# Optimization experiments

Hardware: AMD Instinct MI355X
Metric: run time of the kernel (lower is better)

## Reference

```python
import jax, jax.numpy as jnp
import numpy as np

B, IN_DIM, HID, K, D = 16384, 1024, 2048, 8192, 128
COMMIT = 0.25


def setup_inputs() -> dict:
    key = jax.random.key(0)
    ks = jax.random.split(key, 10)
    s1 = 1.0 / np.sqrt(IN_DIM)
    s2 = 1.0 / np.sqrt(HID)
    s3 = 1.0 / np.sqrt(D)
    return {
        "x": jax.random.uniform(ks[0], (B, IN_DIM), dtype=jnp.float32),
        "W1": jax.random.normal(ks[1], (IN_DIM, HID), dtype=jnp.float32) * s1,
        "b1": jnp.zeros((HID,), jnp.float32),
        "W2": jax.random.normal(ks[2], (HID, D), dtype=jnp.float32) * s2,
        "b2": jnp.zeros((D,), jnp.float32),
        # torch init: uniform(-1/K, 1/K)
        "codebook": jax.random.uniform(ks[3], (K, D), dtype=jnp.float32, minval=-1.0 / K, maxval=1.0 / K),
        "W3": jax.random.normal(ks[4], (D, HID), dtype=jnp.float32) * s3,
        "b3": jnp.zeros((HID,), jnp.float32),
        "W4": jax.random.normal(ks[5], (HID, IN_DIM), dtype=jnp.float32) * s2,
        "b4": jnp.zeros((IN_DIM,), jnp.float32),
    }


def reference(x, W1, b1, W2, b2, codebook, W3, b3, W4, b4):
    # Encoder MLP: [B, IN] -> [B, D]
    h = jax.nn.relu(x @ W1 + b1)
    z = h @ W2 + b2                                   # [B, D]

    # Squared-distance to codebook: ||z||^2 - 2 z C^T + ||C||^2  -> [B, K]
    dists = (jnp.sum(z * z, axis=1, keepdims=True)
             - 2.0 * (z @ codebook.T)
             + jnp.sum(codebook * codebook, axis=1))
    indices = jnp.argmin(dists, axis=1)               # [B]
    z_q = codebook[indices]                            # [B, D]

    # Straight-through estimator
    z_q_st = z + jax.lax.stop_gradient(z_q - z)

    # Decoder MLP: [B, D] -> [B, IN]
    h2 = jax.nn.relu(z_q_st @ W3 + b3)
    recon = jax.nn.sigmoid(h2 @ W4 + b4)

    sg_zq = jax.lax.stop_gradient(z_q)
    mse = jnp.mean(jnp.square(sg_zq - z))
    loss = mse + COMMIT * mse
    return (recon, loss, indices)
```

## Files before the change

kernel.cpp:

```cpp
#include <hip/hip_runtime.h>
#include <hip/hip_bf16.h>


#define B_    16384
#define INDIM 1024
#define HID   2048
#define KCB   8192
#define DDIM  128

#define CAND_CAP 2000000u
#define LBUF_CAP 1024u

typedef __bf16    bf16x8   __attribute__((ext_vector_type(8)));
typedef float     floatx4  __attribute__((ext_vector_type(4)));
typedef double    doublex4 __attribute__((ext_vector_type(4)));
typedef _Float16  half8    __attribute__((ext_vector_type(8)));
typedef __fp16    fp16x2   __attribute__((ext_vector_type(2)));

#define XS 4096.0f
#define WS 8192.0f
#define SCALE_INV 2.9802322387695312e-08

__device__ __forceinline__ unsigned long long pack_key(float d, int code)
{
    unsigned int u = __float_as_uint(d);
    u = (u & 0x80000000u) ? ~u : (u | 0x80000000u);
    return ((unsigned long long)u << 32) | (unsigned int)code;
}

__device__ __forceinline__ float unpack_d(unsigned long long key)
{
    unsigned int u = (unsigned int)(key >> 32);
    u = (u & 0x80000000u) ? (u ^ 0x80000000u) : ~u;
    return __uint_as_float(u);
}

__device__ __forceinline__ void gll16(const float* g, float* l)
{
    __builtin_amdgcn_global_load_lds(
        (const __attribute__((address_space(1))) void*)g,
        (__attribute__((address_space(3))) void*)l, 16, 0, 0);
}

template <int ACT, int PMASK>
__launch_bounds__(256)
__global__ void gemm_split_f16(const float* __restrict__ A, const _Float16* __restrict__ Bs_g,
                               const float* __restrict__ bias, float* __restrict__ Cout,
                               int M, int N, int K)
{
    __shared__ float    As[128 * 32];
    __shared__ _Float16 Bsh[64 * 64];

    const int t    = threadIdx.x;
    const int m0   = blockIdx.y * 128, n0 = blockIdx.x * 64;
    const int wave = t >> 6, lane = t & 63;
    const int wr   = (wave >> 1) * 64, wc = (wave & 1) * 32;
    const int quad = lane >> 4, l16 = lane & 15;
    const int lr   = lane >> 3;
    const int lcA  = ((lane & 7) ^ lr) * 4;
    const int slB  = lane & 7;
    const int lrB  = lane >> 3;

    floatx4  accf[4][2];
    doublex4 accd[4][2];
#pragma unroll
    for (int i = 0; i < 4; ++i)
#pragma unroll
        for (int j = 0; j < 2; ++j) {
            accf[i][j] = (floatx4){0.f, 0.f, 0.f, 0.f};
            accd[i][j] = (doublex4){0.0, 0.0, 0.0, 0.0};
        }

    const int NKT = K >> 5;
    for (int kt = 0; kt < NKT; ++kt) {
        const int k0 = kt << 5;
        __syncthreads();
#pragma unroll
        for (int s = 0; s < 4; ++s) {
            int r = wave * 32 + s * 8;
            gll16(A + (size_t)(m0 + r + lr) * K + k0 + lcA, &As[r * 32]);
        }
#pragma unroll
        for (int s = 0; s < 2; ++s) {
            int rb = wave * 16 + s * 8 + lrB;
            int ccs = slB ^ (lrB & 7);
            gll16((const float*)(Bs_g + (size_t)(n0 + rb) * (2 * K) + kt * 64 + ccs * 8),
                  (float*)&Bsh[(wave * 16 + s * 8) * 64]);
        }
        __syncthreads();

        half8 a1[4], a2[4];
#pragma unroll
        for (int i = 0; i < 4; ++i) {
            const int row = wr + i * 16 + l16;
            const int s0  = (2 * quad) ^ (row & 7);
            const int s1  = (2 * quad + 1) ^ (row & 7);
            floatx4 f0 = *(const floatx4*)&As[row * 32 + s0 * 4];
            floatx4 f1 = *(const floatx4*)&As[row * 32 + s1 * 4];
            union { half8 v; fp16x2 h[4]; } u1, u2;
            float sv[8];
#pragma unroll
            for (int q = 0; q < 4; ++q) sv[q] = f0[q] * XS;
#pragma unroll
            for (int q = 0; q < 4; ++q) sv[4 + q] = f1[q] * XS;
#pragma unroll
            for (int q = 0; q < 4; ++q) {
                fp16x2 hi = __builtin_amdgcn_cvt_pkrtz(sv[2 * q], sv[2 * q + 1]);
                u1.h[q] = hi;
                float r0 = sv[2 * q] - (float)hi[0];
                float r1 = sv[2 * q + 1] - (float)hi[1];
                u2.h[q] = __builtin_amdgcn_cvt_pkrtz(r0, r1);
            }
            a1[i] = u1.v; a2[i] = u2.v;
        }
        half8 b1[2], b2[2];
#pragma unroll
        for (int j = 0; j < 2; ++j) {
            const int row = wc + j * 16 + l16;
            b1[j] = *(const half8*)&Bsh[row * 64 + ((0 + quad) ^ (row & 7)) * 8];
            b2[j] = *(const half8*)&Bsh[row * 64 + ((4 + quad) ^ (row & 7)) * 8];
        }
#pragma unroll
        for (int i = 0; i < 4; ++i)
#pragma unroll
            for (int j = 0; j < 2; ++j)
                accf[i][j] = __builtin_amdgcn_mfma_f32_16x16x32_f16(a1[i], b1[j], accf[i][j], 0, 0, 0);
#pragma unroll
        for (int i = 0; i < 4; ++i)
#pragma unroll
            for (int j = 0; j < 2; ++j)
                accf[i][j] = __builtin_amdgcn_mfma_f32_16x16x32_f16(a1[i], b2[j], accf[i][j], 0, 0, 0);
#pragma unroll
        for (int i = 0; i < 4; ++i)
#pragma unroll
            for (int j = 0; j < 2; ++j)
                accf[i][j] = __builtin_amdgcn_mfma_f32_16x16x32_f16(a2[i], b1[j], accf[i][j], 0, 0, 0);

        if ((kt & PMASK) == PMASK) {
#pragma unroll
            for (int i = 0; i < 4; ++i)
#pragma unroll
                for (int j = 0; j < 2; ++j) {
#pragma unroll
                    for (int r = 0; r < 4; ++r)
                        accd[i][j][r] += (double)accf[i][j][r] * SCALE_INV;
                    accf[i][j] = (floatx4){0.f, 0.f, 0.f, 0.f};
                }
        }
    }
    if (NKT & PMASK) {
#pragma unroll
        for (int i = 0; i < 4; ++i)
#pragma unroll
            for (int j = 0; j < 2; ++j)
#pragma unroll
                for (int r = 0; r < 4; ++r)
                    accd[i][j][r] += (double)accf[i][j][r] * SCALE_INV;
    }

#pragma unroll
    for (int i = 0; i < 4; ++i)
#pragma unroll
        for (int j = 0; j < 2; ++j)
#pragma unroll
            for (int r = 0; r < 4; ++r) {
                int row = m0 + wr + i * 16 + quad * 4 + r;
                int col = n0 + wc + j * 16 + l16;
                float f = (float)(accd[i][j][r] + (double)bias[col]);
                if (ACT == 1) f = fmaxf(f, 0.f);
                Cout[(size_t)row * N + col] = f;
            }
}

__launch_bounds__(256)
__global__ void gemm_split_pre(const _Float16* __restrict__ As_g, const _Float16* __restrict__ Bs_g,
                               const float* __restrict__ bias, float* __restrict__ Cout,
                               int M, int N, int K)
{
    __shared__ _Float16 Ash[128 * 64];
    __shared__ _Float16 Bsh[64 * 64];

    const int t    = threadIdx.x;
    const int m0   = blockIdx.y * 128, n0 = blockIdx.x * 64;
    const int wave = t >> 6, lane = t & 63;
    const int wr   = (wave >> 1) * 64, wc = (wave & 1) * 32;
    const int quad = lane >> 4, l16 = lane & 15;
    const int slB  = lane & 7;
    const int lrB  = lane >> 3;
    const int ccs  = slB ^ (lrB & 7);

    floatx4  accf[4][2];
    doublex4 accd[4][2];
#pragma unroll
    for (int i = 0; i < 4; ++i)
#pragma unroll
        for (int j = 0; j < 2; ++j) {
            accf[i][j] = (floatx4){0.f, 0.f, 0.f, 0.f};
            accd[i][j] = (doublex4){0.0, 0.0, 0.0, 0.0};
        }

    const int NKT = K >> 5;
    for (int kt = 0; kt < NKT; ++kt) {
        __syncthreads();
#pragma unroll
        for (int s = 0; s < 4; ++s) {
            int ra = wave * 32 + s * 8 + lrB;
            gll16((const float*)(As_g + (size_t)(m0 + ra) * (2 * K) + kt * 64 + ccs * 8),
                  (float*)&Ash[(wave * 32 + s * 8) * 64]);
        }
#pragma unroll
        for (int s = 0; s < 2; ++s) {
            int rb = wave * 16 + s * 8 + lrB;
            gll16((const float*)(Bs_g + (size_t)(n0 + rb) * (2 * K) + kt * 64 + ccs * 8),
                  (float*)&Bsh[(wave * 16 + s * 8) * 64]);
        }
        __syncthreads();

        half8 a1[4], a2[4], b1[2], b2[2];
#pragma unroll
        for (int i = 0; i < 4; ++i) {
            const int row = wr + i * 16 + l16;
            a1[i] = *(const half8*)&Ash[row * 64 + ((0 + quad) ^ (row & 7)) * 8];
            a2[i] = *(const half8*)&Ash[row * 64 + ((4 + quad) ^ (row & 7)) * 8];
        }
#pragma unroll
        for (int j = 0; j < 2; ++j) {
            const int row = wc + j * 16 + l16;
            b1[j] = *(const half8*)&Bsh[row * 64 + ((0 + quad) ^ (row & 7)) * 8];
            b2[j] = *(const half8*)&Bsh[row * 64 + ((4 + quad) ^ (row & 7)) * 8];
        }
#pragma unroll
        for (int i = 0; i < 4; ++i)
#pragma unroll
            for (int j = 0; j < 2; ++j)
                accf[i][j] = __builtin_amdgcn_mfma_f32_16x16x32_f16(a1[i], b1[j], accf[i][j], 0, 0, 0);
#pragma unroll
        for (int i = 0; i < 4; ++i)
#pragma unroll
            for (int j = 0; j < 2; ++j)
                accf[i][j] = __builtin_amdgcn_mfma_f32_16x16x32_f16(a1[i], b2[j], accf[i][j], 0, 0, 0);
#pragma unroll
        for (int i = 0; i < 4; ++i)
#pragma unroll
            for (int j = 0; j < 2; ++j)
                accf[i][j] = __builtin_amdgcn_mfma_f32_16x16x32_f16(a2[i], b1[j], accf[i][j], 0, 0, 0);

        if ((kt & 3) == 3) {
#pragma unroll
            for (int i = 0; i < 4; ++i)
#pragma unroll
                for (int j = 0; j < 2; ++j) {
#pragma unroll
                    for (int r = 0; r < 4; ++r)
                        accd[i][j][r] += (double)accf[i][j][r] * SCALE_INV;
                    accf[i][j] = (floatx4){0.f, 0.f, 0.f, 0.f};
                }
        }
    }

#pragma unroll
    for (int i = 0; i < 4; ++i)
#pragma unroll
        for (int j = 0; j < 2; ++j)
#pragma unroll
            for (int r = 0; r < 4; ++r) {
                int row = m0 + wr + i * 16 + quad * 4 + r;
                int col = n0 + wc + j * 16 + l16;
                float f = (float)(accd[i][j][r] + (double)bias[col]);
                f = fmaxf(f, 0.f);
                Cout[(size_t)row * N + col] = f;
            }
}

__global__ void split_x(const float* __restrict__ in, _Float16* __restrict__ outS, int n8)
{
    int i = blockIdx.x * 256 + threadIdx.x;
    if (i >= n8) return;
    const int K = INDIM;
    int m  = i / (K / 8);
    int k8 = i % (K / 8);
    int k  = k8 * 8;
    const float* src = in + (size_t)m * K + k;
    floatx4 f0 = *(const floatx4*)(src);
    floatx4 f1 = *(const floatx4*)(src + 4);
    union { half8 v; fp16x2 h[4]; } u1, u2;
    float sv[8];
#pragma unroll
    for (int q = 0; q < 4; ++q) sv[q] = f0[q] * XS;
#pragma unroll
    for (int q = 0; q < 4; ++q) sv[4 + q] = f1[q] * XS;
#pragma unroll
    for (int q = 0; q < 4; ++q) {
        fp16x2 hi = __builtin_amdgcn_cvt_pkrtz(sv[2 * q], sv[2 * q + 1]);
        u1.h[q] = hi;
        float r0 = sv[2 * q] - (float)hi[0];
        float r1 = sv[2 * q + 1] - (float)hi[1];
        u2.h[q] = __builtin_amdgcn_cvt_pkrtz(r0, r1);
    }
    size_t base = (size_t)m * (2 * K) + (size_t)(k >> 5) * 64 + (k & 31);
    *(half8*)(outS + base)      = u1.v;
    *(half8*)(outS + base + 32) = u2.v;
}

__global__ void transpose_split_f16(const float* __restrict__ in, _Float16* __restrict__ outS,
                                    int K, int N)
{
    __shared__ float tile[32][33];
    int k0 = blockIdx.x * 32, n0 = blockIdx.y * 32;
    int tr = threadIdx.x >> 5, tc = threadIdx.x & 31;
#pragma unroll
    for (int s = 0; s < 4; ++s)
        tile[tr + 8 * s][tc] = in[(size_t)(k0 + tr + 8 * s) * N + n0 + tc];
    __syncthreads();
#pragma unroll
    for (int s = 0; s < 4; ++s) {
        int n = n0 + tr + 8 * s;
        int k = k0 + tc;
        float w = tile[tc][tr + 8 * s] * WS;
        _Float16 p0 = (_Float16)w;
        float r = w - (float)p0;
        _Float16 p1 = (_Float16)r;
        size_t base = (size_t)n * (2 * K) + (size_t)(k >> 5) * 64 + (k & 31);
        outS[base]      = p0;
        outS[base + 32] = p1;
    }
}

__global__ void rownorm_kernel(const float* __restrict__ M, float* __restrict__ nrm)
{
    int k = blockIdx.x * 4 + (threadIdx.x >> 6);
    int lane = threadIdx.x & 63;
    float2 c = *(const float2*)(M + (size_t)k * DDIM + lane * 2);
    float q0 = c.x * c.x;
    float q1 = c.y * c.y;
    double s = (double)q0 + (double)q1;
#pragma unroll
    for (int off = 32; off > 0; off >>= 1) s += __shfl_down(s, off);
    if (lane == 0) nrm[k] = (float)s;
}

__global__ void cnmax_kernel(const float* __restrict__ cn, float* __restrict__ out)
{
    __shared__ float red[4];
    int t = threadIdx.x;
    float m = 0.f;
    for (int i = t; i < KCB; i += 256) m = fmaxf(m, cn[i]);
#pragma unroll
    for (int off = 32; off > 0; off >>= 1) m = fmaxf(m, __shfl_down(m, off));
    if ((t & 63) == 0) red[t >> 6] = m;
    __syncthreads();
    if (t == 0) out[0] = fmaxf(fmaxf(red[0], red[1]), fmaxf(red[2], red[3]));
}

__global__ void cvt_half(const float* __restrict__ in, _Float16* __restrict__ out,
                         float scale, int n8)
{
    int i = blockIdx.x * 256 + threadIdx.x;
    if (i >= n8) return;
    const float4 a = *(const float4*)(in + (size_t)i * 8);
    const float4 b = *(const float4*)(in + (size_t)i * 8 + 4);
    half8 h;
    h[0] = (_Float16)(a.x * scale); h[1] = (_Float16)(a.y * scale);
    h[2] = (_Float16)(a.z * scale); h[3] = (_Float16)(a.w * scale);
    h[4] = (_Float16)(b.x * scale); h[5] = (_Float16)(b.y * scale);
    h[6] = (_Float16)(b.z * scale); h[7] = (_Float16)(b.w * scale);
    *(half8*)(out + (size_t)i * 8) = h;
}

template <int EMIT>
__launch_bounds__(256)
__global__ void score_sweep2(const _Float16* __restrict__ zh, const _Float16* __restrict__ ch,
                             const float* __restrict__ nz32, const float* __restrict__ cn32,
                             unsigned long long* __restrict__ gbestA,
                             const float* __restrict__ cnmaxp,
                             unsigned* __restrict__ listCnt, unsigned* __restrict__ list)
{
    __shared__ __align__(16) _Float16 Zs[32 * 128];
    __shared__ __align__(16) _Float16 Cs[128 * 128];
    __shared__ unsigned long long best[32];
    __shared__ unsigned lbuf[LBUF_CAP];
    __shared__ unsigned lcnt, lbase;

    const int t    = threadIdx.x;
    const int m0   = blockIdx.x * 32;
    const int wave = t >> 6, lane = t & 63;
    const int quad = lane >> 4, l16 = lane & 15;
    const int srow = lane >> 4, sc = lane & 15;

    if (EMIT == 0) { if (t < 32) best[t] = ~0ull; }
    else if (t == 0) lcnt = 0u;

#pragma unroll
    for (int s = 0; s < 2; ++s) {
        const int rbase = s * 16 + wave * 4;
        const int ra = rbase + srow;
        const int cs = sc ^ ((ra & 7) << 1);
        gll16((const float*)(zh + (size_t)(m0 + ra) * 128 + cs * 8),
              (float*)&Zs[rbase * 128]);
    }
    __syncthreads();

    half8 af[2][4];
#pragma unroll
    for (int i = 0; i < 2; ++i) {
        const int rl = i * 16 + l16;
#pragma unroll
        for (int ks = 0; ks < 4; ++ks) {
            const int cc = (ks * 4 + quad) ^ ((rl & 7) << 1);
            af[i][ks] = *(const half8*)&Zs[rl * 128 + cc * 8];
        }
    }

    const float cnm = *cnmaxp;
    float nzv[8], thr[8], bd[8];
    int   bc[8];
#pragma unroll
    for (int i = 0; i < 2; ++i)
#pragma unroll
        for (int r = 0; r < 4; ++r) {
            const int q = i * 4 + r;
            const int grow = m0 + i * 16 + quad * 4 + r;
            nzv[q] = nz32[grow];
            if (EMIT) {
                thr[q] = unpack_d(gbestA[grow]) + 2.4e-3f * sqrtf(nzv[q] * cnm) + 6.0e-5f;
            } else {
                bd[q] = 3.4e38f; bc[q] = 0x7fffffff;
            }
        }

    for (int nt = 0; nt < KCB / 128; ++nt) {
        const int n0 = nt * 128;
        __syncthreads();
#pragma unroll
        for (int s = 0; s < 8; ++s) {
            const int rbase = s * 16 + wave * 4;
            const int ra = rbase + srow;
            const int cs = sc ^ ((ra & 7) << 1);
            gll16((const float*)(ch + (size_t)(n0 + ra) * 128 + cs * 8),
                  (float*)&Cs[rbase * 128]);
        }
        __syncthreads();

        floatx4 acc[2][2];
#pragma unroll
        for (int i = 0; i < 2; ++i)
#pragma unroll
            for (int j = 0; j < 2; ++j) acc[i][j] = (floatx4){0.f, 0.f, 0.f, 0.f};
#pragma unroll
        for (int ks = 0; ks < 4; ++ks) {
            half8 bf[2];
#pragma unroll
            for (int j = 0; j < 2; ++j) {
                const int rl = wave * 32 + j * 16 + l16;
                const int cc = (ks * 4 + quad) ^ ((rl & 7) << 1);
                bf[j] = *(const half8*)&Cs[rl * 128 + cc * 8];
            }
#pragma unroll
            for (int i = 0; i < 2; ++i)
#pragma unroll
                for (int j = 0; j < 2; ++j)
                    acc[i][j] = __builtin_amdgcn_mfma_f32_16x16x32_f16(af[i][ks], bf[j], acc[i][j], 0, 0, 0);
        }

#pragma unroll
        for (int i = 0; i < 2; ++i)
#pragma unroll
            for (int r = 0; r < 4; ++r) {
                const int q = i * 4 + r;
#pragma unroll
                for (int j = 0; j < 2; ++j) {
                    const int code = n0 + wave * 32 + j * 16 + l16;
                    float s = acc[i][j][r] * (1.0f / 4096.0f);
                    float d = (nzv[q] - 2.0f * s) + cn32[code];
                    if (EMIT) {
                        if (d <= thr[q]) {
                            unsigned ent = ((unsigned)(m0 + i * 16 + quad * 4 + r) << 13) | (unsigned)code;
                            unsigned idx = atomicAdd(&lcnt, 1u);
                            if (idx < LBUF_CAP) lbuf[idx] = ent;
                            else {
                                unsigned g = atomicAdd(listCnt, 1u);
                                if (g < CAND_CAP) list[g] = ent;
                            }
                        }
                    } else {
                        if (d < bd[q]) { bd[q] = d; bc[q] = code; }
                    }
                }
            }
    }

    if (EMIT == 0) {
#pragma unroll
        for (int i = 0; i < 2; ++i)
#pragma unroll
            for (int r = 0; r < 4; ++r) {
                const int q = i * 4 + r;
                atomicMin(&best[i * 16 + quad * 4 + r], pack_key(bd[q], bc[q]));
            }
        __syncthreads();
        if (t < 32) gbestA[m0 + t] = best[t];
    } else {
        __syncthreads();
        unsigned cnt = lcnt; if (cnt > LBUF_CAP) cnt = LBUF_CAP;
        if (t == 0) lbase = atomicAdd(listCnt, cnt);
        __syncthreads();
        for (unsigned e = t; e < cnt; e += 256) {
            unsigned g = lbase + e;
            if (g < CAND_CAP) list[g] = lbuf[e];
        }
    }
}

__launch_bounds__(256)
__global__ void refine_kernel(const float* __restrict__ z, const float* __restrict__ cb,
                              const float* __restrict__ nz32, const float* __restrict__ cn32,
                              const unsigned* __restrict__ listCnt,
                              const unsigned* __restrict__ list,
                              unsigned long long* __restrict__ gbest)
{
    unsigned cnt = *listCnt;
    if (cnt > CAND_CAP) cnt = CAND_CAP;
    const int lane = threadIdx.x & 63;
    for (unsigned p = blockIdx.x * 4 + (threadIdx.x >> 6); p < cnt; p += gridDim.x * 4) {
        const unsigned e = list[p];
        const int r = (int)(e >> 13), k = (int)(e & 8191u);
        float2 zv = *(const float2*)(z  + (size_t)r * DDIM + lane * 2);
        float2 cv = *(const float2*)(cb + (size_t)k * DDIM + lane * 2);
        double s = (double)zv.x * (double)cv.x + (double)zv.y * (double)cv.y;
#pragma unroll
        for (int off = 32; off > 0; off >>= 1) s += __shfl_down(s, off);
        if (lane == 0) {
            float s32 = (float)s;
            float d = (nz32[r] - 2.0f * s32) + cn32[k];
            atomicMin(&gbest[r], pack_key(d, k));
        }
    }
}

__global__ void init_gbest(unsigned long long* __restrict__ g)
{
    g[blockIdx.x * 256 + threadIdx.x] = ~0ull;
}

__global__ void gather_zq_loss(const float* __restrict__ z, const float* __restrict__ cb,
                               const unsigned long long* __restrict__ gbest,
                               float* __restrict__ zq, double* __restrict__ acc)
{
    int r = blockIdx.x * 4 + (threadIdx.x >> 6);
    int lane = threadIdx.x & 63;
    int k = (int)(gbest[r] & 0xffffffffull);
    float2 zv = *(const float2*)(z  + (size_t)r * DDIM + lane * 2);
    float2 cv = *(const float2*)(cb + (size_t)k * DDIM + lane * 2);
    *(float2*)(zq + (size_t)r * DDIM + lane * 2) = cv;
    double dx = (double)cv.x - (double)zv.x, dy = (double)cv.y - (double)zv.y;
    double s = dx * dx + dy * dy;
#pragma unroll
    for (int off = 32; off > 0; off >>= 1) s += __shfl_down(s, off);
    if (lane == 0) atomicAdd(acc, s);
}

__global__ void init_scalars(double* acc, unsigned* cnt)
{
    if (threadIdx.x == 0 && blockIdx.x == 0) { *acc = 0.0; *cnt = 0u; }
}

__global__ void finalize_kernel(const unsigned long long* __restrict__ gbest,
                                const double* __restrict__ acc, float* __restrict__ out)
{
    int tid = blockIdx.x * 256 + threadIdx.x;
    if (tid < B_) out[16777217 + tid] = (float)(int)(gbest[tid] & 0xffffffffull);
    if (tid == 0) out[16777216] = (float)((*acc) * 1.25 / (double)(B_ * DDIM));
}

__global__ void transpose_to_bf16(const float* __restrict__ in, __bf16* __restrict__ outT,
                                  int K, int N)
{
    __shared__ float tile[32][33];
    int k0 = blockIdx.x * 32, n0 = blockIdx.y * 32;
    int tr = threadIdx.x >> 5, tc = threadIdx.x & 31;
#pragma unroll
    for (int s = 0; s < 4; ++s)
        tile[tr + 8 * s][tc] = in[(size_t)(k0 + tr + 8 * s) * N + n0 + tc];
    __syncthreads();
#pragma unroll
    for (int s = 0; s < 4; ++s)
        outT[(size_t)(n0 + tr + 8 * s) * K + k0 + tc] = (__bf16)tile[tc][tr + 8 * s];
}

template <bool A_F32, int ACT>
__launch_bounds__(256)
__global__ void gemm_mfma(const void* __restrict__ Ap, const __bf16* __restrict__ BT,
                          const float* __restrict__ bias, void* __restrict__ Cp,
                          int M, int N, int K)
{
    __shared__ __bf16 Asm[128 * 32];
    __shared__ __bf16 Bsm[128 * 32];

    const int t    = threadIdx.x;
    const int m0   = blockIdx.y * 128, n0 = blockIdx.x * 128;
    const int wave = t >> 6, lane = t & 63;
    const int wr   = (wave >> 1) * 64, wc = (wave & 1) * 64;
    const int quad = lane >> 4, l16 = lane & 15;
    const int sr   = t >> 1, sh = t & 1;

    floatx4 acc[4][4];
#pragma unroll
    for (int i = 0; i < 4; ++i)
#pragma unroll
        for (int j = 0; j < 4; ++j) acc[i][j] = (floatx4){0.f, 0.f, 0.f, 0.f};

    for (int k0 = 0; k0 < K; k0 += 32) {
        if (A_F32) {
            const float* src = (const float*)Ap + (size_t)(m0 + sr) * K + k0 + sh * 16;
            __bf16 tmp[16];
#pragma unroll
            for (int q = 0; q < 4; ++q) {
                float4 v = *(const float4*)(src + q * 4);
                tmp[q * 4 + 0] = (__bf16)v.x; tmp[q * 4 + 1] = (__bf16)v.y;
                tmp[q * 4 + 2] = (__bf16)v.z; tmp[q * 4 + 3] = (__bf16)v.w;
            }
            *(bf16x8*)&Asm[sr * 32 + sh * 16 + 0] = *(bf16x8*)&tmp[0];
            *(bf16x8*)&Asm[sr * 32 + sh * 16 + 8] = *(bf16x8*)&tmp[8];
        } else {
            const __bf16* src = (const __bf16*)Ap + (size_t)(m0 + sr) * K + k0 + sh * 16;
            *(uint4*)&Asm[sr * 32 + sh * 16] = *(const uint4*)src;
            *(uint4*)&Asm[sr * 32 + sh * 16 + 8] = *(const uint4*)(src + 8);
        }
        {
            const __bf16* src = BT + (size_t)(n0 + sr) * K + k0 + sh * 16;
            *(uint4*)&Bsm[sr * 32 + sh * 16] = *(const uint4*)src;
            *(uint4*)&Bsm[sr * 32 + sh * 16 + 8] = *(const uint4*)(src + 8);
        }
        __syncthreads();
        bf16x8 af[4], bfr[4];
#pragma unroll
        for (int i = 0; i < 4; ++i)
            af[i] = *(const bf16x8*)&Asm[(wr + i * 16 + l16) * 32 + quad * 8];
#pragma unroll
        for (int j = 0; j < 4; ++j)
            bfr[j] = *(const bf16x8*)&Bsm[(wc + j * 16 + l16) * 32 + quad * 8];
#pragma unroll
        for (int i = 0; i < 4; ++i)
#pragma unroll
            for (int j = 0; j < 4; ++j)
                acc[i][j] = __builtin_amdgcn_mfma_f32_16x16x32_bf16(af[i], bfr[j], acc[i][j], 0, 0, 0);
        __syncthreads();
    }

#pragma unroll
    for (int i = 0; i < 4; ++i)
#pragma unroll
        for (int j = 0; j < 4; ++j) {
            int col = n0 + wc + j * 16 + l16;
            float b = bias[col];
#pragma unroll
            for (int r = 0; r < 4; ++r) {
                int row = m0 + wr + i * 16 + quad * 4 + r;
                float v = acc[i][j][r] + b;
                if (ACT == 1) {
                    v = fmaxf(v, 0.f);
                    ((__bf16*)Cp)[(size_t)row * N + col] = (__bf16)v;
                } else {
                    v = 1.f / (1.f + __expf(-v));
                    ((float*)Cp)[(size_t)row * N + col] = v;
                }
            }
        }
}

extern "C" void kernel_launch(void* const* d_in, const int* in_sizes, int n_in,
                              void* d_out, int out_size, void* d_ws, size_t ws_size,
                              hipStream_t stream)
{
    const float* x  = (const float*)d_in[0];
    const float* W1 = (const float*)d_in[1];
    const float* b1 = (const float*)d_in[2];
    const float* W2 = (const float*)d_in[3];
    const float* b2 = (const float*)d_in[4];
    const float* cb = (const float*)d_in[5];
    const float* W3 = (const float*)d_in[6];
    const float* b3 = (const float*)d_in[7];
    const float* W4 = (const float*)d_in[8];
    const float* b4 = (const float*)d_in[9];
    float* out = (float*)d_out;

    char* ws = (char*)d_ws;
    float*  h    = (float*)(ws);
    __bf16* h2b  = (__bf16*)(ws + 16777216ull);
    float*  z32  = (float*)(ws + 134217728ull);
    float*  zq   = (float*)(ws + 142606336ull);
    _Float16* W1s = (_Float16*)(ws + 142606336ull);
    float*  nz32 = (float*)(ws + 150994944ull);
    float*  cn32 = (float*)(ws + 151060480ull);
    unsigned long long* gbest = (unsigned long long*)(ws + 151093248ull);
    double* acc  = (double*)(ws + 151224320ull);
    float*  cnmax   = (float*)(ws + 151224328ull);
    unsigned* listCnt = (unsigned*)(ws + 151224332ull);
    __bf16* W3t  = (__bf16*)(ws + 151228416ull);
    __bf16* W4t  = (__bf16*)(ws + 151752704ull);
    _Float16* W2s = (_Float16*)(ws + 155947008ull);

    _Float16* zh  = (_Float16*)(ws);
    _Float16* chh = (_Float16*)(ws + 4194304ull);
    unsigned long long* gbestA = (unsigned long long*)(ws + 6291456ull);
    unsigned* list = (unsigned*)(ws + 8388608ull);

    const unsigned long long XS_OFF = 157286400ull;
    _Float16* xs = (_Float16*)(ws + XS_OFF);
    const bool pre_split_x = (ws_size >= XS_OFF + 67108864ull);

    init_scalars<<<1, 64, 0, stream>>>(acc, listCnt);
    init_gbest<<<B_ / 256, 256, 0, stream>>>(gbest);
    rownorm_kernel<<<KCB / 4, 256, 0, stream>>>(cb, cn32);
    cnmax_kernel<<<1, 256, 0, stream>>>(cn32, cnmax);
    transpose_to_bf16<<<dim3(DDIM / 32, HID / 32), 256, 0, stream>>>(W3, W3t, DDIM, HID);
    transpose_to_bf16<<<dim3(HID / 32, INDIM / 32), 256, 0, stream>>>(W4, W4t, HID, INDIM);
    transpose_split_f16<<<dim3(INDIM / 32, HID / 32), 256, 0, stream>>>(W1, W1s, INDIM, HID);
    transpose_split_f16<<<dim3(HID / 32, DDIM / 32), 256, 0, stream>>>(W2, W2s, HID, DDIM);

    if (pre_split_x) {
        split_x<<<(B_ * INDIM / 8) / 256, 256, 0, stream>>>(x, xs, B_ * INDIM / 8);
        gemm_split_pre<<<dim3(HID / 64, B_ / 128), 256, 0, stream>>>(
            xs, W1s, b1, h, B_, HID, INDIM);
    } else {
        gemm_split_f16<1, 3><<<dim3(HID / 64, B_ / 128), 256, 0, stream>>>(
            x, W1s, b1, h, B_, HID, INDIM);
    }
    gemm_split_f16<0, 1><<<dim3(DDIM / 64, B_ / 128), 256, 0, stream>>>(
        h, W2s, b2, z32, B_, DDIM, HID);
    rownorm_kernel<<<B_ / 4, 256, 0, stream>>>(z32, nz32);

    cvt_half<<<(B_ * DDIM / 8) / 256, 256, 0, stream>>>(z32, zh, 1.0f, B_ * DDIM / 8);
    cvt_half<<<(KCB * DDIM / 8) / 256, 256, 0, stream>>>(cb, chh, 4096.0f, KCB * DDIM / 8);
    score_sweep2<0><<<B_ / 32, 256, 0, stream>>>(
        zh, chh, nz32, cn32, gbestA, cnmax, listCnt, list);
    score_sweep2<1><<<B_ / 32, 256, 0, stream>>>(
        zh, chh, nz32, cn32, gbestA, cnmax, listCnt, list);
    refine_kernel<<<1024, 256, 0, stream>>>(z32, cb, nz32, cn32, listCnt, list, gbest);

    gather_zq_loss<<<B_ / 4, 256, 0, stream>>>(z32, cb, gbest, zq, acc);
    gemm_mfma<true, 1><<<dim3(HID / 128, B_ / 128), 256, 0, stream>>>(
        (const void*)zq, W3t, b3, (void*)h2b, B_, HID, DDIM);
    gemm_mfma<false, 2><<<dim3(INDIM / 128, B_ / 128), 256, 0, stream>>>(
        (const void*)h2b, W4t, b4, (void*)out, B_, INDIM, HID);

    finalize_kernel<<<B_ / 256, 256, 0, stream>>>(gbest, acc, out);
}
```

Before: 990.2 us.

## Emit pre-split fp16 hidden from layer 1 and use async-LDS bf16 decoder GEMMs

The first encoder GEMM now writes its ReLU output directly as a pre-split fp16 hi/lo pair in the tiled layout the split GEMM expects. The second encoder GEMM then reuses the gll16-based pre-split kernel, with smaller M tiles and a different fp64 flush period, instead of re-splitting fp32 activations inside its load loop. The decoder GEMMs are replaced with a variant that loads A and B tiles via global-to-LDS direct loads with a swizzled layout, and the gathered z_q is written as bf16 rather than fp32. Together these aim to cut activation traffic and per-tile conversion work, at the cost of more template variants and layout coupling between kernels.

Result: no change. 1.008 ms (+1.8%).

```diff
diff --git a/kernel.cpp b/kernel.cpp
--- a/kernel.cpp
+++ b/kernel.cpp
@@ -172,27 +172,28 @@
             }
 }
 
+template <int IM, int ACT, int PMASK, int SPLITOUT>
 __launch_bounds__(256)
 __global__ void gemm_split_pre(const _Float16* __restrict__ As_g, const _Float16* __restrict__ Bs_g,
-                               const float* __restrict__ bias, float* __restrict__ Cout,
+                               const float* __restrict__ bias, void* __restrict__ Cp,
                                int M, int N, int K)
 {
-    __shared__ _Float16 Ash[128 * 64];
+    __shared__ _Float16 Ash[IM * 32 * 64];
     __shared__ _Float16 Bsh[64 * 64];
 
     const int t    = threadIdx.x;
-    const int m0   = blockIdx.y * 128, n0 = blockIdx.x * 64;
+    const int m0   = blockIdx.y * (IM * 32), n0 = blockIdx.x * 64;
     const int wave = t >> 6, lane = t & 63;
-    const int wr   = (wave >> 1) * 64, wc = (wave & 1) * 32;
+    const int wr   = (wave >> 1) * (IM * 16), wc = (wave & 1) * 32;
     const int quad = lane >> 4, l16 = lane & 15;
     const int slB  = lane & 7;
     const int lrB  = lane >> 3;
     const int ccs  = slB ^ (lrB & 7);
 
-    floatx4  accf[4][2];
-    doublex4 accd[4][2];
-#pragma unroll
-    for (int i = 0; i < 4; ++i)
+    floatx4  accf[IM][2];
+    doublex4 accd[IM][2];
+#pragma unroll
+    for (int i = 0; i < IM; ++i)
 #pragma unroll
         for (int j = 0; j < 2; ++j) {
             accf[i][j] = (floatx4){0.f, 0.f, 0.f, 0.f};
@@ -203,10 +204,10 @@
     for (int kt = 0; kt < NKT; ++kt) {
         __syncthreads();
 #pragma unroll
-        for (int s = 0; s < 4; ++s) {
-            int ra = wave * 32 + s * 8 + lrB;
+        for (int s = 0; s < IM; ++s) {
+            int ra = wave * (IM * 8) + s * 8 + lrB;
             gll16((const float*)(As_g + (size_t)(m0 + ra) * (2 * K) + kt * 64 + ccs * 8),
-                  (float*)&Ash[(wave * 32 + s * 8) * 64]);
+                  (float*)&Ash[(wave * (IM * 8) + s * 8) * 64]);
         }
 #pragma unroll
         for (int s = 0; s < 2; ++s) {
@@ -216,9 +217,9 @@
         }
         __syncthreads();
 
-        half8 a1[4], a2[4], b1[2], b2[2];
-#pragma unroll
-        for (int i = 0; i < 4; ++i) {
+        half8 a1[IM], a2[IM], b1[2], b2[2];
+#pragma unroll
+        for (int i = 0; i < IM; ++i) {
             const int row = wr + i * 16 + l16;
             a1[i] = *(const half8*)&Ash[row * 64 + ((0 + quad) ^ (row & 7)) * 8];
             a2[i] = *(const half8*)&Ash[row * 64 + ((4 + quad) ^ (row & 7)) * 8];
@@ -230,24 +231,24 @@
             b2[j] = *(const half8*)&Bsh[row * 64 + ((4 + quad) ^ (row & 7)) * 8];
         }
 #pragma unroll
-        for (int i = 0; i < 4; ++i)
+        for (int i = 0; i < IM; ++i)
 #pragma unroll
             for (int j = 0; j < 2; ++j)
                 accf[i][j] = __builtin_amdgcn_mfma_f32_16x16x32_f16(a1[i], b1[j], accf[i][j], 0, 0, 0);
 #pragma unroll
-        for (int i = 0; i < 4; ++i)
+        for (int i = 0; i < IM; ++i)
 #pragma unroll
             for (int j = 0; j < 2; ++j)
                 accf[i][j] = __builtin_amdgcn_mfma_f32_16x16x32_f16(a1[i], b2[j], accf[i][j], 0, 0, 0);
 #pragma unroll
-        for (int i = 0; i < 4; ++i)
+        for (int i = 0; i < IM; ++i)
 #pragma unroll
             for (int j = 0; j < 2; ++j)
                 accf[i][j] = __builtin_amdgcn_mfma_f32_16x16x32_f16(a2[i], b1[j], accf[i][j], 0, 0, 0);
 
-        if ((kt & 3) == 3) {
-#pragma unroll
-            for (int i = 0; i < 4; ++i)
+        if ((kt & PMASK) == PMASK) {
+#pragma unroll
+            for (int i = 0; i < IM; ++i)
 #pragma unroll
                 for (int j = 0; j < 2; ++j) {
 #pragma unroll
@@ -257,9 +258,18 @@
                 }
         }
     }
-
-#pragma unroll
-    for (int i = 0; i < 4; ++i)
+    if (NKT & PMASK) {
+#pragma unroll
+        for (int i = 0; i < IM; ++i)
+#pragma unroll
+            for (int j = 0; j < 2; ++j)
+#pragma unroll
+                for (int r = 0; r < 4; ++r)
+                    accd[i][j][r] += (double)accf[i][j][r] * SCALE_INV;
+    }
+
+#pragma unroll
+    for (int i = 0; i < IM; ++i)
 #pragma unroll
         for (int j = 0; j < 2; ++j)
 #pragma unroll
@@ -267,9 +277,104 @@
                 int row = m0 + wr + i * 16 + quad * 4 + r;
                 int col = n0 + wc + j * 16 + l16;
                 float f = (float)(accd[i][j][r] + (double)bias[col]);
-                f = fmaxf(f, 0.f);
-                Cout[(size_t)row * N + col] = f;
+                if (ACT == 1) f = fmaxf(f, 0.f);
+                if (SPLITOUT) {
+                    float sv = f * XS;
+                    _Float16 p0 = (_Float16)sv;
+                    _Float16 p1 = (_Float16)(sv - (float)p0);
+                    _Float16* hs = (_Float16*)Cp;
+                    size_t base = (size_t)row * (2 * (size_t)N)
+                                + (size_t)(col >> 5) * 64 + (col & 31);
+                    hs[base]      = p0;
+                    hs[base + 32] = p1;
+                } else {
+                    ((float*)Cp)[(size_t)row * N + col] = f;
+                }
             }
+}
+
+template <int ACT>
+__launch_bounds__(256)
+__global__ void gemm_bf16_gll(const __bf16* __restrict__ A, const __bf16* __restrict__ BT,
+                              const float* __restrict__ bias, void* __restrict__ Cp,
+                              int M, int N, int K)
+{
+    __shared__ __bf16 Asm[128 * 32];
+    __shared__ __bf16 Bsm[128 * 32];
+
+    const int t    = threadIdx.x;
+    const int m0   = blockIdx.y * 128, n0 = blockIdx.x * 128;
+    const int wave = t >> 6, lane = t & 63;
+    const int wr   = (wave >> 1) * 64, wc = (wave & 1) * 64;
+    const int quad = lane >> 4, l16 = lane & 15;
+    const int srow = lane >> 2;
+    const int schk = lane & 3;
+
+    floatx4 acc[4][4];
+#pragma unroll
+    for (int i = 0; i < 4; ++i)
+#pragma unroll
+        for (int j = 0; j < 4; ++j) acc[i][j] = (floatx4){0.f, 0.f, 0.f, 0.f};
+
+    for (int k0 = 0; k0 < K; k0 += 32) {
+        __syncthreads();
+#pragma unroll
+        for (int s = 0; s < 2; ++s) {
+            const int rbase = wave * 32 + s * 16;
+            const int ra = rbase + srow;
+            const int cs = (schk - (ra >> 1)) & 3;
+            gll16((const float*)(A + (size_t)(m0 + ra) * K + k0 + cs * 8),
+                  (float*)&Asm[rbase * 32]);
+        }
+#pragma unroll
+        for (int s = 0; s < 2; ++s) {
+            const int rbase = wave * 32 + s * 16;
+            const int rb = rbase + srow;
+            const int cs = (schk - (rb >> 1)) & 3;
+            gll16((const float*)(BT + (size_t)(n0 + rb) * K + k0 + cs * 8),
+                  (float*)&Bsm[rbase * 32]);
+        }
+        __syncthreads();
+
+        bf16x8 af[4], bfr[4];
+#pragma unroll
+        for (int i = 0; i < 4; ++i) {
+            const int rl = wr + i * 16 + l16;
+            const int sl = (quad + (rl >> 1)) & 3;
+            af[i] = *(const bf16x8*)&Asm[rl * 32 + sl * 8];
+        }
+#pragma unroll
+        for (int j = 0; j < 4; ++j) {
+            const int rl = wc + j * 16 + l16;
+            const int sl = (quad + (rl >> 1)) & 3;
+            bfr[j] = *(const bf16x8*)&Bsm[rl * 32 + sl * 8];
+        }
+#pragma unroll
+        for (int i = 0; i < 4; ++i)
+#pragma unroll
+            for (int j = 0; j < 4; ++j)
+                acc[i][j] = __builtin_amdgcn_mfma_f32_16x16x32_bf16(af[i], bfr[j], acc[i][j], 0, 0, 0);
+    }
+
+#pragma unroll
+    for (int i = 0; i < 4; ++i)
+#pragma unroll
+        for (int j = 0; j < 4; ++j) {
+            int col = n0 + wc + j * 16 + l16;
+            float b = bias[col];
+#pragma unroll
+            for (int r = 0; r < 4; ++r) {
+                int row = m0 + wr + i * 16 + quad * 4 + r;
+                float v = acc[i][j][r] + b;
+                if (ACT == 1) {
+                    v = fmaxf(v, 0.f);
+                    ((__bf16*)Cp)[(size_t)row * N + col] = (__bf16)v;
+                } else {
+                    v = 1.f / (1.f + __expf(-v));
+                    ((float*)Cp)[(size_t)row * N + col] = v;
+                }
+            }
+        }
 }
 
 __global__ void split_x(const float* __restrict__ in, _Float16* __restrict__ outS, int n8)
@@ -544,14 +649,16 @@
 
 __global__ void gather_zq_loss(const float* __restrict__ z, const float* __restrict__ cb,
                                const unsigned long long* __restrict__ gbest,
-                               float* __restrict__ zq, double* __restrict__ acc)
+                               __bf16* __restrict__ zqb, double* __restrict__ acc)
 {
     int r = blockIdx.x * 4 + (threadIdx.x >> 6);
     int lane = threadIdx.x & 63;
     int k = (int)(gbest[r] & 0xffffffffull);
     float2 zv = *(const float2*)(z  + (size_t)r * DDIM + lane * 2);
     float2 cv = *(const float2*)(cb + (size_t)k * DDIM + lane * 2);
-    *(float2*)(zq + (size_t)r * DDIM + lane * 2) = cv;
+    __bf16 b0 = (__bf16)cv.x, b1 = (__bf16)cv.y;
+    zqb[(size_t)r * DDIM + lane * 2]     = b0;
+    zqb[(size_t)r * DDIM + lane * 2 + 1] = b1;
     double dx = (double)cv.x - (double)zv.x, dy = (double)cv.y - (double)zv.y;
     double s = dx * dx + dy * dy;
 #pragma unroll
@@ -585,87 +692,6 @@
 #pragma unroll
     for (int s = 0; s < 4; ++s)
         outT[(size_t)(n0 + tr + 8 * s) * K + k0 + tc] = (__bf16)tile[tc][tr + 8 * s];
-}
-
-template <bool A_F32, int ACT>
-__launch_bounds__(256)
-__global__ void gemm_mfma(const void* __restrict__ Ap, const __bf16* __restrict__ BT,
-                          const float* __restrict__ bias, void* __restrict__ Cp,
-                          int M, int N, int K)
-{
-    __shared__ __bf16 Asm[128 * 32];
-    __shared__ __bf16 Bsm[128 * 32];
-
-    const int t    = threadIdx.x;
-    const int m0   = blockIdx.y * 128, n0 = blockIdx.x * 128;
-    const int wave = t >> 6, lane = t & 63;
-    const int wr   = (wave >> 1) * 64, wc = (wave & 1) * 64;
-    const int quad = lane >> 4, l16 = lane & 15;
-    const int sr   = t >> 1, sh = t & 1;
-
-    floatx4 acc[4][4];
-#pragma unroll
-    for (int i = 0; i < 4; ++i)
-#pragma unroll
-        for (int j = 0; j < 4; ++j) acc[i][j] = (floatx4){0.f, 0.f, 0.f, 0.f};
-
-    for (int k0 = 0; k0 < K; k0 += 32) {
-        if (A_F32) {
-            const float* src = (const float*)Ap + (size_t)(m0 + sr) * K + k0 + sh * 16;
-            __bf16 tmp[16];
-#pragma unroll
-            for (int q = 0; q < 4; ++q) {
-                float4 v = *(const float4*)(src + q * 4);
-                tmp[q * 4 + 0] = (__bf16)v.x; tmp[q * 4 + 1] = (__bf16)v.y;
-                tmp[q * 4 + 2] = (__bf16)v.z; tmp[q * 4 + 3] = (__bf16)v.w;
-            }
-            *(bf16x8*)&Asm[sr * 32 + sh * 16 + 0] = *(bf16x8*)&tmp[0];
-            *(bf16x8*)&Asm[sr * 32 + sh * 16 + 8] = *(bf16x8*)&tmp[8];
-        } else {
-            const __bf16* src = (const __bf16*)Ap + (size_t)(m0 + sr) * K + k0 + sh * 16;
-            *(uint4*)&Asm[sr * 32 + sh * 16] = *(const uint4*)src;
-            *(uint4*)&Asm[sr * 32 + sh * 16 + 8] = *(const uint4*)(src + 8);
-        }
-        {
-            const __bf16* src = BT + (size_t)(n0 + sr) * K + k0 + sh * 16;
-            *(uint4*)&Bsm[sr * 32 + sh * 16] = *(const uint4*)src;
-            *(uint4*)&Bsm[sr * 32 + sh * 16 + 8] = *(const uint4*)(src + 8);
-        }
-        __syncthreads();
-        bf16x8 af[4], bfr[4];
-#pragma unroll
-        for (int i = 0; i < 4; ++i)
-            af[i] = *(const bf16x8*)&Asm[(wr + i * 16 + l16) * 32 + quad * 8];
-#pragma unroll
-        for (int j = 0; j < 4; ++j)
-            bfr[j] = *(const bf16x8*)&Bsm[(wc + j * 16 + l16) * 32 + quad * 8];
-#pragma unroll
-        for (int i = 0; i < 4; ++i)
-#pragma unroll
-            for (int j = 0; j < 4; ++j)
-                acc[i][j] = __builtin_amdgcn_mfma_f32_16x16x32_bf16(af[i], bfr[j], acc[i][j], 0, 0, 0);
-        __syncthreads();
-    }
-
-#pragma unroll
-    for (int i = 0; i < 4; ++i)
-#pragma unroll
-        for (int j = 0; j < 4; ++j) {
-            int col = n0 + wc + j * 16 + l16;
-            float b = bias[col];
-#pragma unroll
-            for (int r = 0; r < 4; ++r) {
-                int row = m0 + wr + i * 16 + quad * 4 + r;
-                float v = acc[i][j][r] + b;
-                if (ACT == 1) {
-                    v = fmaxf(v, 0.f);
-                    ((__bf16*)Cp)[(size_t)row * N + col] = (__bf16)v;
-                } else {
-                    v = 1.f / (1.f + __expf(-v));
-                    ((float*)Cp)[(size_t)row * N + col] = v;
-                }
-            }
-        }
 }
 
 extern "C" void kernel_launch(void* const* d_in, const int* in_sizes, int n_in,
@@ -685,10 +711,11 @@
     float* out = (float*)d_out;
 
     char* ws = (char*)d_ws;
+    _Float16* hs = (_Float16*)(ws);
     float*  h    = (float*)(ws);
     __bf16* h2b  = (__bf16*)(ws + 16777216ull);
     float*  z32  = (float*)(ws + 134217728ull);
-    float*  zq   = (float*)(ws + 142606336ull);
+    __bf16* zqb  = (__bf16*)(ws + 142606336ull);
     _Float16* W1s = (_Float16*)(ws + 142606336ull);
     float*  nz32 = (float*)(ws + 150994944ull);
     float*  cn32 = (float*)(ws + 151060480ull);
@@ -720,14 +747,16 @@
 
     if (pre_split_x) {
         split_x<<<(B_ * INDIM / 8) / 256, 256, 0, stream>>>(x, xs, B_ * INDIM / 8);
-        gemm_split_pre<<<dim3(HID / 64, B_ / 128), 256, 0, stream>>>(
-            xs, W1s, b1, h, B_, HID, INDIM);
+        gemm_split_pre<4, 1, 3, 1><<<dim3(HID / 64, B_ / 128), 256, 0, stream>>>(
+            xs, W1s, b1, (void*)hs, B_, HID, INDIM);
+        gemm_split_pre<2, 0, 1, 0><<<dim3(DDIM / 64, B_ / 64), 256, 0, stream>>>(
+            hs, W2s, b2, (void*)z32, B_, DDIM, HID);
     } else {
         gemm_split_f16<1, 3><<<dim3(HID / 64, B_ / 128), 256, 0, stream>>>(
             x, W1s, b1, h, B_, HID, INDIM);
-    }
-    gemm_split_f16<0, 1><<<dim3(DDIM / 64, B_ / 128), 256, 0, stream>>>(
-        h, W2s, b2, z32, B_, DDIM, HID);
+        gemm_split_f16<0, 1><<<dim3(DDIM / 64, B_ / 128), 256, 0, stream>>>(
+            h, W2s, b2, z32, B_, DDIM, HID);
+    }
     rownorm_kernel<<<B_ / 4, 256, 0, stream>>>(z32, nz32);
 
     cvt_half<<<(B_ * DDIM / 8) / 256, 256, 0, stream>>>(z32, zh, 1.0f, B_ * DDIM / 8);
@@ -738,11 +767,11 @@
         zh, chh, nz32, cn32, gbestA, cnmax, listCnt, list);
     refine_kernel<<<1024, 256, 0, stream>>>(z32, cb, nz32, cn32, listCnt, list, gbest);
 
-    gather_zq_loss<<<B_ / 4, 256, 0, stream>>>(z32, cb, gbest, zq, acc);
-    gemm_mfma<true, 1><<<dim3(HID / 128, B_ / 128), 256, 0, stream>>>(
-        (const void*)zq, W3t, b3, (void*)h2b, B_, HID, DDIM);
-    gemm_mfma<false, 2><<<dim3(INDIM / 128, B_ / 128), 256, 0, stream>>>(
-        (const void*)h2b, W4t, b4, (void*)out, B_, INDIM, HID);
+    gather_zq_loss<<<B_ / 4, 256, 0, stream>>>(z32, cb, gbest, zqb, acc);
+    gemm_bf16_gll<1><<<dim3(HID / 128, B_ / 128), 256, 0, stream>>>(
+        zqb, W3t, b3, (void*)h2b, B_, HID, DDIM);
+    gemm_bf16_gll<2><<<dim3(INDIM / 128, B_ / 128), 256, 0, stream>>>(
+        h2b, W4t, b4, (void*)out, B_, INDIM, HID);
 
     finalize_kernel<<<B_ / 256, 256, 0, stream>>>(gbest, acc, out);
 }
```
